# Optimization experiments

Measured on AMD Instinct MI355X. Metric: run time of the kernel, lower is better.

Reference implementation:

```python
import jax, jax.numpy as jnp
import numpy as np

DIM = 768
HEADS = 4
NUM_L1 = 16
NUM_L2 = 64
BATCH = 128


def _ln(x, g, b, eps=1e-5):
    m = x.mean(-1, keepdims=True)
    v = x.var(-1, keepdims=True)
    return (x - m) / jnp.sqrt(v + eps) * g + b


def _cluster_attn(x, wq, wk, wv, fcw, fcb, g, b):
    # x: [B, 2, D]; wq/wk/wv: [H*D, D] torch-Linear layout; fcw: [D, H*D]
    B, S, D = x.shape
    H = HEADS
    q = jnp.einsum('bsd,hed->bhse', x, wq.reshape(H, D, D))
    k = jnp.einsum('bsd,hed->bhse', x, wk.reshape(H, D, D))
    v = jnp.einsum('bsd,hed->bhse', x, wv.reshape(H, D, D))
    attn = jax.nn.softmax(jnp.einsum('bhse,bhte->bhst', q, k) / jnp.sqrt(jnp.float32(D)), axis=-1)
    o = jnp.einsum('bhst,bhte->bhse', attn, v)          # [B, H, S, D]
    o = o.transpose(0, 2, 1, 3).reshape(B, S, H * D)     # [B, S, H*D]
    o = o @ fcw.T + fcb                                  # [B, S, D]
    return _ln(o + x, g, b)


def _score_level(tokens, task_p, wq, wk, wv, fcw, fcb, g, b, sg, sb, sw, sbias):
    # tokens: [1, T, D]; task_p: [batch, 1, D]
    bsz = task_p.shape[0]
    T = tokens.shape[1]
    tok = jnp.broadcast_to(tokens, (bsz, T, DIM))
    tp = jnp.broadcast_to(task_p, (bsz, T, DIM))
    combined = jnp.stack([tok, tp], axis=2).reshape(bsz * T, 2, DIM)
    att = _cluster_attn(combined, wq, wk, wv, fcw, fcb, g, b)
    cls = att[:, 0]                                      # [bsz*T, D]
    scores = (_ln(cls, sg, sb) @ sw.T + sbias).reshape(bsz, T)
    return scores


def setup_inputs() -> dict:
    key = jax.random.key(0)
    ks = jax.random.split(key, 32)
    HD = HEADS * DIM

    def n(i, shape, scale):
        return (jax.random.normal(ks[i], shape) * scale).astype(jnp.float32)

    w_std = float(np.sqrt(2.0 / (DIM + DIM)))
    inp = {
        'task_emb': n(0, (BATCH, 1, DIM), 1.0),
        'tokens_l1': n(1, (1, NUM_L1, DIM), 1.0),
        'tokens_l2': n(2, (1, NUM_L2, DIM), 1.0),
        'task_proj_w': n(3, (DIM, DIM), w_std),
        'task_proj_b': jnp.zeros((DIM,), jnp.float32),
        'wq1': n(4, (HD, DIM), w_std), 'wk1': n(5, (HD, DIM), w_std), 'wv1': n(6, (HD, DIM), w_std),
        'fcw1': n(7, (DIM, HD), float(np.sqrt(2.0 / (DIM + HD)))),
        'fcb1': jnp.zeros((DIM,), jnp.float32),
        'lng1': jnp.ones((DIM,), jnp.float32), 'lnb1': jnp.zeros((DIM,), jnp.float32),
        'slng1': jnp.ones((DIM,), jnp.float32), 'slnb1': jnp.zeros((DIM,), jnp.float32),
        'sw1': n(8, (1, DIM), w_std), 'sb1': jnp.zeros((1,), jnp.float32),
        'wq2': n(9, (HD, DIM), w_std), 'wk2': n(10, (HD, DIM), w_std), 'wv2': n(11, (HD, DIM), w_std),
        'fcw2': n(12, (DIM, HD), float(np.sqrt(2.0 / (DIM + HD)))),
        'fcb2': jnp.zeros((DIM,), jnp.float32),
        'lng2': jnp.ones((DIM,), jnp.float32), 'lnb2': jnp.zeros((DIM,), jnp.float32),
        'slng2': jnp.ones((DIM,), jnp.float32), 'slnb2': jnp.zeros((DIM,), jnp.float32),
        'sw2': n(13, (1, DIM), w_std), 'sb2': jnp.zeros((1,), jnp.float32),
    }
    return inp


def reference(task_emb, tokens_l1, tokens_l2, task_proj_w, task_proj_b,
              wq1, wk1, wv1, fcw1, fcb1, lng1, lnb1, slng1, slnb1, sw1, sb1,
              wq2, wk2, wv2, fcw2, fcb2, lng2, lnb2, slng2, slnb2, sw2, sb2):
    # shared task projection (self.task_proj)
    task_p = task_emb @ task_proj_w.T + task_proj_b    # [batch, 1, D]
    l1 = _score_level(tokens_l1, task_p, wq1, wk1, wv1, fcw1, fcb1, lng1, lnb1, slng1, slnb1, sw1, sb1)
    l2 = _score_level(tokens_l2, task_p, wq2, wk2, wv2, fcw2, fcb2, lng2, lnb2, slng2, slnb2, sw2, sb2)
    return jnp.concatenate([l1, l2], axis=-1)           # [batch, NUM_L1 + NUM_L2]
```

## Files before the change

### kernel.cpp

```cpp
#include <hip/hip_runtime.h>
#include <math.h>

#define DIM 768
#define HEADS 4
#define HDIM 3072
#define BATCH 128

typedef __attribute__((ext_vector_type(8))) short bfrag;
typedef __attribute__((ext_vector_type(4))) float f32x4;

struct GemmDesc {
    const float* A;
    const float* B;
    const float* bias;
    float* C;
    int lda, ldb, ldc;
    int M, N, K;
    int blockBase;
    int nTiles;
};
#define MAXD 12
struct GemmBatch { GemmDesc d[MAXD]; int nDesc; };

__device__ inline short f2bf(float f) {
    unsigned u = __float_as_uint(f);
    u += 0x7FFF + ((u >> 16) & 1);
    return (short)(u >> 16);
}

__global__ __launch_bounds__(256) void gemm_bf16(GemmBatch batch)
{
    __shared__ __attribute__((aligned(16))) short Asl[2][2048];
    __shared__ __attribute__((aligned(16))) short Bsl[2][8192];

    int bid = blockIdx.x;
    int di = 0;
    while (di + 1 < batch.nDesc && bid >= batch.d[di + 1].blockBase) ++di;
    const GemmDesc g = batch.d[di];
    int lb = bid - g.blockBase;
    int mt = lb / g.nTiles;
    int nt = lb - mt * g.nTiles;
    const int m0 = mt * 32, n0 = nt * 128;
    const int M = g.M, lda = g.lda, ldb = g.ldb;
    const float* __restrict__ A = g.A;
    const float* __restrict__ B = g.B;

    const int tid = threadIdx.x;
    const int lane = tid & 63;
    const int w = tid >> 6;

    int aoff[2]; bool aok[2];
#pragma unroll
    for (int ia = 0; ia < 2; ++ia) {
        int S = tid + 256 * ia;
        int reg = S >> 7, h = S & 127, l = h >> 1, j2 = h & 1;
        int mg = reg >> 1, kb = reg & 1;
        int m = mg * 16 + (l & 15);
        int k = kb * 32 + (l >> 4) * 8 + j2 * 4;
        aok[ia] = (m0 + m) < M;
        aoff[ia] = (m0 + m) * lda + k;
    }
    int boff[8];
#pragma unroll
    for (int ib = 0; ib < 8; ++ib) {
        int S = tid + 256 * ib;
        int reg = S >> 7, h = S & 127, l = h >> 1, j2 = h & 1;
        int ng = reg >> 1, kb = reg & 1;
        int n = ng * 16 + (l & 15);
        int k = kb * 32 + (l >> 4) * 8 + j2 * 4;
        boff[ib] = (n0 + n) * ldb + k;
    }

    float4 pa[2], pb[8];
    const float4 fz = { 0.f, 0.f, 0.f, 0.f };

    auto LOADT = [&](int k0) {
#pragma unroll
        for (int ia = 0; ia < 2; ++ia)
            pa[ia] = aok[ia] ? *(const float4*)(A + aoff[ia] + k0) : fz;
#pragma unroll
        for (int ib = 0; ib < 8; ++ib)
            pb[ib] = *(const float4*)(B + boff[ib] + k0);
    };
    auto WRITET = [&](int bf) {
#pragma unroll
        for (int ia = 0; ia < 2; ++ia) {
            short4 s;
            s.x = f2bf(pa[ia].x); s.y = f2bf(pa[ia].y);
            s.z = f2bf(pa[ia].z); s.w = f2bf(pa[ia].w);
            *(short4*)&Asl[bf][(tid + 256 * ia) * 4] = s;
        }
#pragma unroll
        for (int ib = 0; ib < 8; ++ib) {
            short4 s;
            s.x = f2bf(pb[ib].x); s.y = f2bf(pb[ib].y);
            s.z = f2bf(pb[ib].z); s.w = f2bf(pb[ib].w);
            *(short4*)&Bsl[bf][(tid + 256 * ib) * 4] = s;
        }
    };

    f32x4 acc[2][2];
#pragma unroll
    for (int a = 0; a < 2; ++a)
#pragma unroll
        for (int b = 0; b < 2; ++b) acc[a][b] = (f32x4){0.f, 0.f, 0.f, 0.f};

    const int nk = g.K >> 6;
    LOADT(0);
    WRITET(0);
    __syncthreads();

    int buf = 0;
    for (int t = 0; t < nk; ++t) {
        bool more = (t + 1 < nk);
        if (more) LOADT((t + 1) << 6);
#pragma unroll
        for (int kb = 0; kb < 2; ++kb) {
            bfrag a0 = *(const bfrag*)&Asl[buf][(0 * 2 + kb) * 512 + lane * 8];
            bfrag a1 = *(const bfrag*)&Asl[buf][(1 * 2 + kb) * 512 + lane * 8];
            bfrag b0 = *(const bfrag*)&Bsl[buf][((w * 2 + 0) * 2 + kb) * 512 + lane * 8];
            bfrag b1 = *(const bfrag*)&Bsl[buf][((w * 2 + 1) * 2 + kb) * 512 + lane * 8];
            acc[0][0] = __builtin_amdgcn_mfma_f32_16x16x32_bf16(a0, b0, acc[0][0], 0, 0, 0);
            acc[0][1] = __builtin_amdgcn_mfma_f32_16x16x32_bf16(a0, b1, acc[0][1], 0, 0, 0);
            acc[1][0] = __builtin_amdgcn_mfma_f32_16x16x32_bf16(a1, b0, acc[1][0], 0, 0, 0);
            acc[1][1] = __builtin_amdgcn_mfma_f32_16x16x32_bf16(a1, b1, acc[1][1], 0, 0, 0);
        }
        if (more) WRITET(buf ^ 1);
        __syncthreads();
        buf ^= 1;
    }

    const int gq = lane >> 4;
    const int cn = lane & 15;
#pragma unroll
    for (int fn = 0; fn < 2; ++fn) {
        int n = n0 + w * 32 + fn * 16 + cn;
        float bv = g.bias ? g.bias[n] : 0.f;
#pragma unroll
        for (int fm = 0; fm < 2; ++fm) {
#pragma unroll
            for (int r = 0; r < 4; ++r) {
                int m = m0 + fm * 16 + gq * 4 + r;
                if (m < M) g.C[(long)m * g.ldc + n] = acc[fm][fn][r] + bv;
            }
        }
    }
}

struct ScoreDesc {
    const float *tok_q, *tok_k, *k_task, *U_tok, *U_task, *tokens;
    const float *fcb, *lng, *lnb, *slng, *slnb, *sw, *sbias;
    int T, outOff, blockBase, pad;
};
struct ScoreBatch { ScoreDesc d[2]; };

__device__ inline void block_reduce2(float& a, float& b, float* redA, float* redB, int tid)
{
    int lane = tid & 63, wave = tid >> 6;
#pragma unroll
    for (int off = 32; off; off >>= 1) {
        a += __shfl_down(a, off);
        b += __shfl_down(b, off);
    }
    if (lane == 0) { redA[wave] = a; redB[wave] = b; }
    __syncthreads();
    a = redA[0] + redA[1] + redA[2] + redA[3];
    b = redB[0] + redB[1] + redB[2] + redB[3];
    __syncthreads();
}

__global__ __launch_bounds__(256) void score_kernel(ScoreBatch batch, float* __restrict__ out)
{
    const int si = (blockIdx.x >= batch.d[1].blockBase) ? 1 : 0;
    const ScoreDesc g = batch.d[si];
    const int bid = blockIdx.x - g.blockBase;
    const int T = g.T;
    const int b = bid / T;
    const int t = bid - b * T;
    const int tid = threadIdx.x;
    const int lane = tid & 63;
    const int wave = tid >> 6;

    __shared__ float coef[HEADS][2];
    __shared__ float redA[4], redB[4];

    {
        const float4* q4  = (const float4*)(g.tok_q  + (long)t * HDIM + wave * DIM);
        const float4* kt4 = (const float4*)(g.tok_k  + (long)t * HDIM + wave * DIM);
        const float4* kb4 = (const float4*)(g.k_task + (long)b * HDIM + wave * DIM);
        float s00 = 0.f, s01 = 0.f;
#pragma unroll
        for (int j = 0; j < 3; ++j) {
            int idx = lane + 64 * j;
            float4 qv = q4[idx], kt = kt4[idx], kb = kb4[idx];
            s00 += qv.x * kt.x + qv.y * kt.y + qv.z * kt.z + qv.w * kt.w;
            s01 += qv.x * kb.x + qv.y * kb.y + qv.z * kb.z + qv.w * kb.w;
        }
#pragma unroll
        for (int off = 32; off; off >>= 1) {
            s00 += __shfl_down(s00, off);
            s01 += __shfl_down(s01, off);
        }
        if (lane == 0) {
            const float scale = 0.03608439182435161f;
            float x0 = s00 * scale, x1 = s01 * scale;
            float mx = fmaxf(x0, x1);
            float e0 = expf(x0 - mx), e1 = expf(x1 - mx);
            float inv = 1.f / (e0 + e1);
            coef[wave][0] = e0 * inv;
            coef[wave][1] = e1 * inv;
        }
    }
    __syncthreads();

    const float c00 = coef[0][0], c01 = coef[0][1];
    const float c10 = coef[1][0], c11 = coef[1][1];
    const float c20 = coef[2][0], c21 = coef[2][1];
    const float c30 = coef[3][0], c31 = coef[3][1];

    float r[3];
    float sum = 0.f, sq = 0.f;
    const float* Ut = g.U_tok  + (long)t * HDIM;
    const float* Ub = g.U_task + (long)b * HDIM;
#pragma unroll
    for (int j = 0; j < 3; ++j) {
        int d = tid + j * 256;
        float v = g.fcb[d] + g.tokens[(long)t * DIM + d];
        v += c00 * Ut[d]           + c01 * Ub[d];
        v += c10 * Ut[DIM + d]     + c11 * Ub[DIM + d];
        v += c20 * Ut[2 * DIM + d] + c21 * Ub[2 * DIM + d];
        v += c30 * Ut[3 * DIM + d] + c31 * Ub[3 * DIM + d];
        r[j] = v;
        sum += v;
        sq += v * v;
    }
    block_reduce2(sum, sq, redA, redB, tid);
    float mean = sum * (1.f / DIM);
    float var = sq * (1.f / DIM) - mean * mean;
    float inv = rsqrtf(var + 1e-5f);

    float y[3];
    float sum2 = 0.f, sq2 = 0.f;
#pragma unroll
    for (int j = 0; j < 3; ++j) {
        int d = tid + j * 256;
        float v = (r[j] - mean) * inv * g.lng[d] + g.lnb[d];
        y[j] = v;
        sum2 += v;
        sq2 += v * v;
    }
    block_reduce2(sum2, sq2, redA, redB, tid);
    float mean2 = sum2 * (1.f / DIM);
    float var2 = sq2 * (1.f / DIM) - mean2 * mean2;
    float inv2 = rsqrtf(var2 + 1e-5f);

    float partial = 0.f, dummy = 0.f;
#pragma unroll
    for (int j = 0; j < 3; ++j) {
        int d = tid + j * 256;
        float c = (y[j] - mean2) * inv2 * g.slng[d] + g.slnb[d];
        partial += c * g.sw[d];
    }
    block_reduce2(partial, dummy, redA, redB, tid);
    if (tid == 0) out[(long)b * 80 + g.outOff + t] = partial + g.sbias[0];
}

extern "C" void kernel_launch(void* const* d_in, const int* in_sizes, int n_in,
                              void* d_out, int out_size, void* d_ws, size_t ws_size,
                              hipStream_t stream)
{
    const float* task_emb    = (const float*)d_in[0];
    const float* tokens_l1   = (const float*)d_in[1];
    const float* tokens_l2   = (const float*)d_in[2];
    const float* task_proj_w = (const float*)d_in[3];
    const float* task_proj_b = (const float*)d_in[4];

    const float* wq1  = (const float*)d_in[5];
    const float* wk1  = (const float*)d_in[6];
    const float* wv1  = (const float*)d_in[7];
    const float* fcw1 = (const float*)d_in[8];
    const float* fcb1 = (const float*)d_in[9];
    const float* lng1 = (const float*)d_in[10];
    const float* lnb1 = (const float*)d_in[11];
    const float* slng1= (const float*)d_in[12];
    const float* slnb1= (const float*)d_in[13];
    const float* sw1  = (const float*)d_in[14];
    const float* sb1  = (const float*)d_in[15];

    const float* wq2  = (const float*)d_in[16];
    const float* wk2  = (const float*)d_in[17];
    const float* wv2  = (const float*)d_in[18];
    const float* fcw2 = (const float*)d_in[19];
    const float* fcb2 = (const float*)d_in[20];
    const float* lng2 = (const float*)d_in[21];
    const float* lnb2 = (const float*)d_in[22];
    const float* slng2= (const float*)d_in[23];
    const float* slnb2= (const float*)d_in[24];
    const float* sw2  = (const float*)d_in[25];
    const float* sb2  = (const float*)d_in[26];

    float* out = (float*)d_out;

    float* ws = (float*)d_ws;
    float* task_p   = ws;
    float* tq1      = task_p   +  98304;
    float* tk1      = tq1      +  49152;
    float* tv1      = tk1      +  49152;
    float* ut1      = tv1      +  49152;
    float* tq2      = ut1      +  49152;
    float* tk2      = tq2      + 196608;
    float* tv2      = tk2      + 196608;
    float* ut2      = tv2      + 196608;
    float* ktask1   = ut2      + 196608;
    float* vtask1   = ktask1   + 393216;
    float* utask1   = vtask1   + 393216;
    float* ktask2   = utask1   + 393216;
    float* vtask2   = ktask2   + 393216;
    float* utask2   = vtask2   + 393216;

    auto mkDesc = [](const float* A, int lda, const float* B, int ldb,
                     const float* bias, float* C, int ldc,
                     int M, int N, int K, int base) {
        GemmDesc g;
        g.A = A; g.B = B; g.bias = bias; g.C = C;
        g.lda = lda; g.ldb = ldb; g.ldc = ldc;
        g.M = M; g.N = N; g.K = K;
        g.blockBase = base; g.nTiles = N / 128;
        return g;
    };
    auto blocksOf = [](int M, int N) { return ((M + 31) / 32) * (N / 128); };

    {
        GemmBatch ba; int base = 0, nd = 0;
        ba.d[nd++] = mkDesc(task_emb, DIM, task_proj_w, DIM, task_proj_b,
                            task_p, DIM, BATCH, DIM, DIM, base);
        base += blocksOf(BATCH, DIM);
        const float* tA[2] = { tokens_l1, tokens_l2 };
        int tT[2] = { 16, 64 };
        const float* tW[2][3] = { { wq1, wk1, wv1 }, { wq2, wk2, wv2 } };
        float* tC[2][3] = { { tq1, tk1, tv1 }, { tq2, tk2, tv2 } };
        for (int l = 0; l < 2; ++l)
            for (int w = 0; w < 3; ++w) {
                ba.d[nd++] = mkDesc(tA[l], DIM, tW[l][w], DIM, nullptr,
                                    tC[l][w], HDIM, tT[l], HDIM, DIM, base);
                base += blocksOf(tT[l], HDIM);
            }
        ba.nDesc = nd;
        gemm_bf16<<<dim3(base), dim3(256), 0, stream>>>(ba);
    }

    {
        GemmBatch bb; int base = 0, nd = 0;
        const float* kw[2] = { wk1, wk2 };
        const float* vw[2] = { wv1, wv2 };
        float* kc[2] = { ktask1, ktask2 };
        float* vc[2] = { vtask1, vtask2 };
        for (int l = 0; l < 2; ++l) {
            bb.d[nd++] = mkDesc(task_p, DIM, kw[l], DIM, nullptr,
                                kc[l], HDIM, BATCH, HDIM, DIM, base);
            base += blocksOf(BATCH, HDIM);
            bb.d[nd++] = mkDesc(task_p, DIM, vw[l], DIM, nullptr,
                                vc[l], HDIM, BATCH, HDIM, DIM, base);
            base += blocksOf(BATCH, HDIM);
        }
        const float* fw[2] = { fcw1, fcw2 };
        float* tv[2] = { tv1, tv2 };
        float* ut[2] = { ut1, ut2 };
        int tT[2] = { 16, 64 };
        for (int l = 0; l < 2; ++l)
            for (int h = 0; h < HEADS; ++h) {
                bb.d[nd++] = mkDesc(tv[l] + h * DIM, HDIM, fw[l] + h * DIM, HDIM,
                                    nullptr, ut[l] + h * DIM, HDIM,
                                    tT[l], DIM, DIM, base);
                base += blocksOf(tT[l], DIM);
            }
        bb.nDesc = nd;
        gemm_bf16<<<dim3(base), dim3(256), 0, stream>>>(bb);
    }

    {
        GemmBatch bc; int base = 0, nd = 0;
        const float* fw[2] = { fcw1, fcw2 };
        float* vt[2] = { vtask1, vtask2 };
        float* utk[2] = { utask1, utask2 };
        for (int l = 0; l < 2; ++l)
            for (int h = 0; h < HEADS; ++h) {
                bc.d[nd++] = mkDesc(vt[l] + h * DIM, HDIM, fw[l] + h * DIM, HDIM,
                                    nullptr, utk[l] + h * DIM, HDIM,
                                    BATCH, DIM, DIM, base);
                base += blocksOf(BATCH, DIM);
            }
        bc.nDesc = nd;
        gemm_bf16<<<dim3(base), dim3(256), 0, stream>>>(bc);
    }

    {
        ScoreBatch sb;
        sb.d[0].tok_q = tq1; sb.d[0].tok_k = tk1; sb.d[0].k_task = ktask1;
        sb.d[0].U_tok = ut1; sb.d[0].U_task = utask1; sb.d[0].tokens = tokens_l1;
        sb.d[0].fcb = fcb1; sb.d[0].lng = lng1; sb.d[0].lnb = lnb1;
        sb.d[0].slng = slng1; sb.d[0].slnb = slnb1; sb.d[0].sw = sw1; sb.d[0].sbias = sb1;
        sb.d[0].T = 16; sb.d[0].outOff = 0; sb.d[0].blockBase = 0; sb.d[0].pad = 0;
        sb.d[1].tok_q = tq2; sb.d[1].tok_k = tk2; sb.d[1].k_task = ktask2;
        sb.d[1].U_tok = ut2; sb.d[1].U_task = utask2; sb.d[1].tokens = tokens_l2;
        sb.d[1].fcb = fcb2; sb.d[1].lng = lng2; sb.d[1].lnb = lnb2;
        sb.d[1].slng = slng2; sb.d[1].slnb = slnb2; sb.d[1].sw = sw2; sb.d[1].sbias = sb2;
        sb.d[1].T = 64; sb.d[1].outOff = 16; sb.d[1].blockBase = BATCH * 16; sb.d[1].pad = 0;
        score_kernel<<<dim3(BATCH * 16 + BATCH * 64), dim3(256), 0, stream>>>(sb, out);
    }
}
```

Baseline: 276.7 us.

## Shrink GEMM tile to 32x64 with K-step 32 and hardcoded K loop

```diff
diff --git a/kernel.cpp b/kernel.cpp
--- a/kernel.cpp
+++ b/kernel.cpp
@@ -28,10 +28,16 @@
     return (short)(u >> 16);
 }
 
+#define BAR() do { \
+    asm volatile("s_waitcnt lgkmcnt(0)" ::: "memory"); \
+    __builtin_amdgcn_s_barrier(); \
+    __builtin_amdgcn_sched_barrier(0); \
+} while (0)
+
 __global__ __launch_bounds__(256) void gemm_bf16(GemmBatch batch)
 {
-    __shared__ __attribute__((aligned(16))) short Asl[2][2048];
-    __shared__ __attribute__((aligned(16))) short Bsl[2][8192];
+    __shared__ __attribute__((aligned(16))) short Asl[2][1024];
+    __shared__ __attribute__((aligned(16))) short Bsl[2][2048];
 
     int bid = blockIdx.x;
     int di = 0;
@@ -40,7 +46,7 @@
     int lb = bid - g.blockBase;
     int mt = lb / g.nTiles;
     int nt = lb - mt * g.nTiles;
-    const int m0 = mt * 32, n0 = nt * 128;
+    const int m0 = mt * 32, n0 = nt * 64;
     const int M = g.M, lda = g.lda, ldb = g.ldb;
     const float* __restrict__ A = g.A;
     const float* __restrict__ B = g.B;
@@ -49,102 +55,96 @@
     const int lane = tid & 63;
     const int w = tid >> 6;
 
-    int aoff[2]; bool aok[2];
-#pragma unroll
-    for (int ia = 0; ia < 2; ++ia) {
-        int S = tid + 256 * ia;
-        int reg = S >> 7, h = S & 127, l = h >> 1, j2 = h & 1;
-        int mg = reg >> 1, kb = reg & 1;
-        int m = mg * 16 + (l & 15);
-        int k = kb * 32 + (l >> 4) * 8 + j2 * 4;
-        aok[ia] = (m0 + m) < M;
-        aoff[ia] = (m0 + m) * lda + k;
-    }
-    int boff[8];
-#pragma unroll
-    for (int ib = 0; ib < 8; ++ib) {
-        int S = tid + 256 * ib;
-        int reg = S >> 7, h = S & 127, l = h >> 1, j2 = h & 1;
-        int ng = reg >> 1, kb = reg & 1;
-        int n = ng * 16 + (l & 15);
-        int k = kb * 32 + (l >> 4) * 8 + j2 * 4;
-        boff[ib] = (n0 + n) * ldb + k;
-    }
-
-    float4 pa[2], pb[8];
+    int aoff; bool aok;
+    {
+        int rg = tid >> 7, h = tid & 127, l = h >> 1, j2 = h & 1;
+        int m = rg * 16 + (l & 15);
+        int k = (l >> 4) * 8 + j2 * 4;
+        aok = (m0 + m) < M;
+        aoff = (m0 + m) * lda + k;
+    }
+    int boff0, boff1;
+    {
+        int h = tid & 127, l = h >> 1, j2 = h & 1;
+        int k = (l >> 4) * 8 + j2 * 4;
+        int ng0 = tid >> 7;
+        boff0 = (n0 + ng0 * 16 + (l & 15)) * ldb + k;
+        boff1 = (n0 + (ng0 + 2) * 16 + (l & 15)) * ldb + k;
+    }
+
     const float4 fz = { 0.f, 0.f, 0.f, 0.f };
-
-    auto LOADT = [&](int k0) {
-#pragma unroll
-        for (int ia = 0; ia < 2; ++ia)
-            pa[ia] = aok[ia] ? *(const float4*)(A + aoff[ia] + k0) : fz;
-#pragma unroll
-        for (int ib = 0; ib < 8; ++ib)
-            pb[ib] = *(const float4*)(B + boff[ib] + k0);
-    };
-    auto WRITET = [&](int bf) {
-#pragma unroll
-        for (int ia = 0; ia < 2; ++ia) {
-            short4 s;
-            s.x = f2bf(pa[ia].x); s.y = f2bf(pa[ia].y);
-            s.z = f2bf(pa[ia].z); s.w = f2bf(pa[ia].w);
-            *(short4*)&Asl[bf][(tid + 256 * ia) * 4] = s;
-        }
-#pragma unroll
-        for (int ib = 0; ib < 8; ++ib) {
-            short4 s;
-            s.x = f2bf(pb[ib].x); s.y = f2bf(pb[ib].y);
-            s.z = f2bf(pb[ib].z); s.w = f2bf(pb[ib].w);
-            *(short4*)&Bsl[bf][(tid + 256 * ib) * 4] = s;
-        }
-    };
-
-    f32x4 acc[2][2];
-#pragma unroll
-    for (int a = 0; a < 2; ++a)
-#pragma unroll
-        for (int b = 0; b < 2; ++b) acc[a][b] = (f32x4){0.f, 0.f, 0.f, 0.f};
-
-    const int nk = g.K >> 6;
-    LOADT(0);
-    WRITET(0);
-    __syncthreads();
-
-    int buf = 0;
-    for (int t = 0; t < nk; ++t) {
-        bool more = (t + 1 < nk);
-        if (more) LOADT((t + 1) << 6);
-#pragma unroll
-        for (int kb = 0; kb < 2; ++kb) {
-            bfrag a0 = *(const bfrag*)&Asl[buf][(0 * 2 + kb) * 512 + lane * 8];
-            bfrag a1 = *(const bfrag*)&Asl[buf][(1 * 2 + kb) * 512 + lane * 8];
-            bfrag b0 = *(const bfrag*)&Bsl[buf][((w * 2 + 0) * 2 + kb) * 512 + lane * 8];
-            bfrag b1 = *(const bfrag*)&Bsl[buf][((w * 2 + 1) * 2 + kb) * 512 + lane * 8];
-            acc[0][0] = __builtin_amdgcn_mfma_f32_16x16x32_bf16(a0, b0, acc[0][0], 0, 0, 0);
-            acc[0][1] = __builtin_amdgcn_mfma_f32_16x16x32_bf16(a0, b1, acc[0][1], 0, 0, 0);
-            acc[1][0] = __builtin_amdgcn_mfma_f32_16x16x32_bf16(a1, b0, acc[1][0], 0, 0, 0);
-            acc[1][1] = __builtin_amdgcn_mfma_f32_16x16x32_bf16(a1, b1, acc[1][1], 0, 0, 0);
-        }
-        if (more) WRITET(buf ^ 1);
-        __syncthreads();
-        buf ^= 1;
-    }
+    float4 pa0, pb00, pb01, pa1, pb10, pb11;
+
+#define LOAD0(t) do { int k0 = (t) * 32; \
+    pa0  = aok ? *(const float4*)(A + aoff + k0) : fz; \
+    pb00 = *(const float4*)(B + boff0 + k0); \
+    pb01 = *(const float4*)(B + boff1 + k0); } while (0)
+#define LOAD1(t) do { int k0 = (t) * 32; \
+    pa1  = aok ? *(const float4*)(A + aoff + k0) : fz; \
+    pb10 = *(const float4*)(B + boff0 + k0); \
+    pb11 = *(const float4*)(B + boff1 + k0); } while (0)
+#define CVT(dst, v) do { short4 s_; \
+    s_.x = f2bf((v).x); s_.y = f2bf((v).y); s_.z = f2bf((v).z); s_.w = f2bf((v).w); \
+    *(short4*)(dst) = s_; } while (0)
+#define WRITE0(bf) do { \
+    CVT(&Asl[bf][tid * 4], pa0); \
+    CVT(&Bsl[bf][tid * 4], pb00); \
+    CVT(&Bsl[bf][(tid + 256) * 4], pb01); } while (0)
+#define WRITE1(bf) do { \
+    CVT(&Asl[bf][tid * 4], pa1); \
+    CVT(&Bsl[bf][tid * 4], pb10); \
+    CVT(&Bsl[bf][(tid + 256) * 4], pb11); } while (0)
+
+    f32x4 acc0 = {0.f, 0.f, 0.f, 0.f};
+    f32x4 acc1 = {0.f, 0.f, 0.f, 0.f};
+
+#define COMPUTE(bf) do { \
+    bfrag a0 = *(const bfrag*)&Asl[bf][lane * 8]; \
+    bfrag a1 = *(const bfrag*)&Asl[bf][512 + lane * 8]; \
+    bfrag bb = *(const bfrag*)&Bsl[bf][w * 512 + lane * 8]; \
+    acc0 = __builtin_amdgcn_mfma_f32_16x16x32_bf16(a0, bb, acc0, 0, 0, 0); \
+    acc1 = __builtin_amdgcn_mfma_f32_16x16x32_bf16(a1, bb, acc1, 0, 0, 0); \
+} while (0)
+
+    LOAD0(0); LOAD1(1);
+    WRITE0(0);
+    BAR();
+#pragma unroll 1
+    for (int t = 0; t < 22; t += 2) {
+        LOAD0(t + 2);
+        COMPUTE(0);
+        WRITE1(1);
+        BAR();
+        LOAD1(t + 3);
+        COMPUTE(1);
+        WRITE0(0);
+        BAR();
+    }
+    COMPUTE(0);
+    WRITE1(1);
+    BAR();
+    COMPUTE(1);
 
     const int gq = lane >> 4;
     const int cn = lane & 15;
-#pragma unroll
-    for (int fn = 0; fn < 2; ++fn) {
-        int n = n0 + w * 32 + fn * 16 + cn;
-        float bv = g.bias ? g.bias[n] : 0.f;
-#pragma unroll
-        for (int fm = 0; fm < 2; ++fm) {
-#pragma unroll
-            for (int r = 0; r < 4; ++r) {
-                int m = m0 + fm * 16 + gq * 4 + r;
-                if (m < M) g.C[(long)m * g.ldc + n] = acc[fm][fn][r] + bv;
-            }
-        }
-    }
+    const int n = n0 + w * 16 + cn;
+    float bv = g.bias ? g.bias[n] : 0.f;
+#pragma unroll
+    for (int r = 0; r < 4; ++r) {
+        int m = m0 + gq * 4 + r;
+        if (m < M) g.C[(long)m * g.ldc + n] = acc0[r] + bv;
+    }
+#pragma unroll
+    for (int r = 0; r < 4; ++r) {
+        int m = m0 + 16 + gq * 4 + r;
+        if (m < M) g.C[(long)m * g.ldc + n] = acc1[r] + bv;
+    }
+#undef LOAD0
+#undef LOAD1
+#undef CVT
+#undef WRITE0
+#undef WRITE1
+#undef COMPUTE
 }
 
 struct ScoreDesc {
@@ -325,10 +325,10 @@
         g.A = A; g.B = B; g.bias = bias; g.C = C;
         g.lda = lda; g.ldb = ldb; g.ldc = ldc;
         g.M = M; g.N = N; g.K = K;
-        g.blockBase = base; g.nTiles = N / 128;
+        g.blockBase = base; g.nTiles = N / 64;
         return g;
     };
-    auto blocksOf = [](int M, int N) { return ((M + 31) / 32) * (N / 128); };
+    auto blocksOf = [](int M, int N) { return ((M + 31) / 32) * (N / 64); };
 
     {
         GemmBatch ba; int base = 0, nd = 0;
```

Result: slower. 291.6 us (+5.4%).

## Restructure bf16 GEMM to 16x256 tiles with register-direct B fragments

Applied to the files above, without the earlier changes.

```diff
diff --git a/kernel.cpp b/kernel.cpp
--- a/kernel.cpp
+++ b/kernel.cpp
@@ -1,4 +1,5 @@
 #include <hip/hip_runtime.h>
+#include <hip/hip_bf16.h>
 #include <math.h>
 
 #define DIM 768
@@ -23,15 +24,14 @@
 struct GemmBatch { GemmDesc d[MAXD]; int nDesc; };
 
 __device__ inline short f2bf(float f) {
-    unsigned u = __float_as_uint(f);
-    u += 0x7FFF + ((u >> 16) & 1);
-    return (short)(u >> 16);
-}
-
-__global__ __launch_bounds__(256) void gemm_bf16(GemmBatch batch)
+    union { __hip_bfloat16 h; short s; } u;
+    u.h = __float2bfloat16(f);
+    return u.s;
+}
+
+__global__ __launch_bounds__(256, 4) void gemm_bf16(GemmBatch batch)
 {
-    __shared__ __attribute__((aligned(16))) short Asl[2][2048];
-    __shared__ __attribute__((aligned(16))) short Bsl[2][8192];
+    __shared__ __attribute__((aligned(16))) short Asl[24 * 512];
 
     int bid = blockIdx.x;
     int di = 0;
@@ -40,8 +40,8 @@
     int lb = bid - g.blockBase;
     int mt = lb / g.nTiles;
     int nt = lb - mt * g.nTiles;
-    const int m0 = mt * 32, n0 = nt * 128;
-    const int M = g.M, lda = g.lda, ldb = g.ldb;
+    const int m0 = mt * 16, n0 = nt * 256;
+    const int lda = g.lda, ldb = g.ldb;
     const float* __restrict__ A = g.A;
     const float* __restrict__ B = g.B;
 
@@ -49,100 +49,69 @@
     const int lane = tid & 63;
     const int w = tid >> 6;
 
-    int aoff[2]; bool aok[2];
-#pragma unroll
-    for (int ia = 0; ia < 2; ++ia) {
-        int S = tid + 256 * ia;
-        int reg = S >> 7, h = S & 127, l = h >> 1, j2 = h & 1;
-        int mg = reg >> 1, kb = reg & 1;
-        int m = mg * 16 + (l & 15);
-        int k = kb * 32 + (l >> 4) * 8 + j2 * 4;
-        aok[ia] = (m0 + m) < M;
-        aoff[ia] = (m0 + m) * lda + k;
-    }
-    int boff[8];
-#pragma unroll
-    for (int ib = 0; ib < 8; ++ib) {
-        int S = tid + 256 * ib;
-        int reg = S >> 7, h = S & 127, l = h >> 1, j2 = h & 1;
-        int ng = reg >> 1, kb = reg & 1;
-        int n = ng * 16 + (l & 15);
-        int k = kb * 32 + (l >> 4) * 8 + j2 * 4;
-        boff[ib] = (n0 + n) * ldb + k;
-    }
-
-    float4 pa[2], pb[8];
-    const float4 fz = { 0.f, 0.f, 0.f, 0.f };
-
-    auto LOADT = [&](int k0) {
-#pragma unroll
-        for (int ia = 0; ia < 2; ++ia)
-            pa[ia] = aok[ia] ? *(const float4*)(A + aoff[ia] + k0) : fz;
-#pragma unroll
-        for (int ib = 0; ib < 8; ++ib)
-            pb[ib] = *(const float4*)(B + boff[ib] + k0);
+#pragma unroll
+    for (int i = 0; i < 6; ++i) {
+        int gI = tid + 256 * i;
+        int ks = gI >> 6, l = gI & 63;
+        const float* src = A + (long)(m0 + (l & 15)) * lda + ks * 32 + ((l >> 4) << 3);
+        float4 v0 = *(const float4*)src;
+        float4 v1 = *(const float4*)(src + 4);
+        short4 s0, s1;
+        s0.x = f2bf(v0.x); s0.y = f2bf(v0.y); s0.z = f2bf(v0.z); s0.w = f2bf(v0.w);
+        s1.x = f2bf(v1.x); s1.y = f2bf(v1.y); s1.z = f2bf(v1.z); s1.w = f2bf(v1.w);
+        *(short4*)&Asl[gI * 8]     = s0;
+        *(short4*)&Asl[gI * 8 + 4] = s1;
+    }
+    __syncthreads();
+
+    const float* Bb = B + (long)(n0 + (w << 6) + (lane & 15)) * ldb + ((lane >> 4) << 3);
+
+    f32x4 acc[4];
+#pragma unroll
+    for (int s = 0; s < 4; ++s) acc[s] = (f32x4){0.f, 0.f, 0.f, 0.f};
+
+    float4 P[4][2], Q[4][2];
+
+    auto LD = [&](float4 (&S)[4][2], int ks) {
+#pragma unroll
+        for (int s = 0; s < 4; ++s) {
+            const float* p = Bb + (long)(s * 16) * ldb + ks * 32;
+            S[s][0] = *(const float4*)p;
+            S[s][1] = *(const float4*)(p + 4);
+        }
     };
-    auto WRITET = [&](int bf) {
-#pragma unroll
-        for (int ia = 0; ia < 2; ++ia) {
-            short4 s;
-            s.x = f2bf(pa[ia].x); s.y = f2bf(pa[ia].y);
-            s.z = f2bf(pa[ia].z); s.w = f2bf(pa[ia].w);
-            *(short4*)&Asl[bf][(tid + 256 * ia) * 4] = s;
-        }
-#pragma unroll
-        for (int ib = 0; ib < 8; ++ib) {
-            short4 s;
-            s.x = f2bf(pb[ib].x); s.y = f2bf(pb[ib].y);
-            s.z = f2bf(pb[ib].z); s.w = f2bf(pb[ib].w);
-            *(short4*)&Bsl[bf][(tid + 256 * ib) * 4] = s;
+    auto STEP = [&](float4 (&S)[4][2], int ks) {
+        bfrag af = *(const bfrag*)&Asl[(ks << 9) + (lane << 3)];
+#pragma unroll
+        for (int s = 0; s < 4; ++s) {
+            bfrag bf;
+            bf[0] = f2bf(S[s][0].x); bf[1] = f2bf(S[s][0].y);
+            bf[2] = f2bf(S[s][0].z); bf[3] = f2bf(S[s][0].w);
+            bf[4] = f2bf(S[s][1].x); bf[5] = f2bf(S[s][1].y);
+            bf[6] = f2bf(S[s][1].z); bf[7] = f2bf(S[s][1].w);
+            acc[s] = __builtin_amdgcn_mfma_f32_16x16x32_bf16(af, bf, acc[s], 0, 0, 0);
         }
     };
 
-    f32x4 acc[2][2];
-#pragma unroll
-    for (int a = 0; a < 2; ++a)
-#pragma unroll
-        for (int b = 0; b < 2; ++b) acc[a][b] = (f32x4){0.f, 0.f, 0.f, 0.f};
-
-    const int nk = g.K >> 6;
-    LOADT(0);
-    WRITET(0);
-    __syncthreads();
-
-    int buf = 0;
-    for (int t = 0; t < nk; ++t) {
-        bool more = (t + 1 < nk);
-        if (more) LOADT((t + 1) << 6);
-#pragma unroll
-        for (int kb = 0; kb < 2; ++kb) {
-            bfrag a0 = *(const bfrag*)&Asl[buf][(0 * 2 + kb) * 512 + lane * 8];
-            bfrag a1 = *(const bfrag*)&Asl[buf][(1 * 2 + kb) * 512 + lane * 8];
-            bfrag b0 = *(const bfrag*)&Bsl[buf][((w * 2 + 0) * 2 + kb) * 512 + lane * 8];
-            bfrag b1 = *(const bfrag*)&Bsl[buf][((w * 2 + 1) * 2 + kb) * 512 + lane * 8];
-            acc[0][0] = __builtin_amdgcn_mfma_f32_16x16x32_bf16(a0, b0, acc[0][0], 0, 0, 0);
-            acc[0][1] = __builtin_amdgcn_mfma_f32_16x16x32_bf16(a0, b1, acc[0][1], 0, 0, 0);
-            acc[1][0] = __builtin_amdgcn_mfma_f32_16x16x32_bf16(a1, b0, acc[1][0], 0, 0, 0);
-            acc[1][1] = __builtin_amdgcn_mfma_f32_16x16x32_bf16(a1, b1, acc[1][1], 0, 0, 0);
-        }
-        if (more) WRITET(buf ^ 1);
-        __syncthreads();
-        buf ^= 1;
+    LD(P, 0); LD(Q, 1);
+#pragma unroll
+    for (int ks = 0; ks < 24; ks += 2) {
+        STEP(P, ks);
+        if (ks + 2 < 24) LD(P, ks + 2);
+        STEP(Q, ks + 1);
+        if (ks + 3 < 24) LD(Q, ks + 3);
     }
 
     const int gq = lane >> 4;
     const int cn = lane & 15;
 #pragma unroll
-    for (int fn = 0; fn < 2; ++fn) {
-        int n = n0 + w * 32 + fn * 16 + cn;
+    for (int s = 0; s < 4; ++s) {
+        int n = n0 + (w << 6) + (s << 4) + cn;
         float bv = g.bias ? g.bias[n] : 0.f;
 #pragma unroll
-        for (int fm = 0; fm < 2; ++fm) {
-#pragma unroll
-            for (int r = 0; r < 4; ++r) {
-                int m = m0 + fm * 16 + gq * 4 + r;
-                if (m < M) g.C[(long)m * g.ldc + n] = acc[fm][fn][r] + bv;
-            }
+        for (int r = 0; r < 4; ++r) {
+            int m = m0 + (gq << 2) + r;
+            g.C[(long)m * g.ldc + n] = acc[s][r] + bv;
         }
     }
 }
@@ -325,10 +294,10 @@
         g.A = A; g.B = B; g.bias = bias; g.C = C;
         g.lda = lda; g.ldb = ldb; g.ldc = ldc;
         g.M = M; g.N = N; g.K = K;
-        g.blockBase = base; g.nTiles = N / 128;
+        g.blockBase = base; g.nTiles = N / 256;
         return g;
     };
-    auto blocksOf = [](int M, int N) { return ((M + 31) / 32) * (N / 128); };
+    auto blocksOf = [](int M, int N) { return (M / 16) * (N / 256); };
 
     {
         GemmBatch ba; int base = 0, nd = 0;
```

After: 285.2 us. 1.03x slower.
